# Performance work log

Measured on AMD Instinct MI355X. Metric: run time of the kernel, lower is better.

## Reference

```python
import jax, jax.numpy as jnp
import numpy as np

CHEB_K = 3
DIM_IN = 2
HIDDEN = 64
EMBED_DIM = 10
NODE_NUM = 2048
BATCH = 32


def _gconv(x, supports, W, b, cheb_k=CHEB_K):
    # Chebyshev graph conv applied directly to x (equivalent to building
    # T_k(A) matrices then applying: T_k(A) x = 2 A T_{k-1}(A) x - T_{k-2}(A) x).
    xs = [x, jnp.einsum('nm,bmc->bnc', supports, x)]
    for _ in range(2, cheb_k):
        xs.append(2.0 * jnp.einsum('nm,bmc->bnc', supports, xs[-1]) - xs[-2])
    x_g = jnp.concatenate(xs, axis=-1)          # [B, N, cheb_k*C]
    return jnp.einsum('bni,io->bno', x_g, W) + b


def setup_inputs() -> dict:
    key = jax.random.key(0)
    ks = jax.random.split(key, 7)
    c_in = DIM_IN + HIDDEN                       # 66
    # xavier_normal-ish scale for weights
    def xavier(k, fan_in, fan_out):
        std = float(np.sqrt(2.0 / (fan_in + fan_out)))
        return jax.random.normal(k, (fan_in, fan_out), dtype=jnp.float32) * std
    return {
        'x': jax.random.normal(ks[0], (BATCH, NODE_NUM, DIM_IN), dtype=jnp.float32),
        'state': jax.random.normal(ks[1], (BATCH, NODE_NUM, HIDDEN), dtype=jnp.float32),
        'node_embeddings': jax.random.normal(ks[2], (NODE_NUM, EMBED_DIM), dtype=jnp.float32),
        'W_gate': xavier(ks[3], CHEB_K * c_in, 2 * HIDDEN),
        'b_gate': jnp.zeros((2 * HIDDEN,), dtype=jnp.float32),
        'W_update': xavier(ks[4], CHEB_K * c_in, HIDDEN),
        'b_update': jnp.zeros((HIDDEN,), dtype=jnp.float32),
    }


def reference(x, state, node_embeddings, W_gate, b_gate, W_update, b_update):
    # adaptive adjacency: softmax(relu(E E^T), axis=1)
    logits = jnp.einsum('nc,mc->nm', node_embeddings, node_embeddings)
    supports = jax.nn.softmax(jax.nn.relu(logits), axis=1)   # [N, N]

    input_and_state = jnp.concatenate([x, state], axis=-1)   # [B, N, dim_in+hidden]
    z_r = jax.nn.sigmoid(_gconv(input_and_state, supports, W_gate, b_gate))
    z, r = jnp.split(z_r, 2, axis=-1)                        # each [B, N, hidden]
    candidate = jnp.concatenate([x, z * state], axis=-1)
    hc = jnp.tanh(_gconv(candidate, supports, W_update, b_update))
    h = r * state + (1.0 - r) * hc
    return h
```

## Files before the change

kernel.cpp:

```cpp
#include <hip/hip_runtime.h>


typedef __bf16 bf16x8 __attribute__((ext_vector_type(8)));
typedef __bf16 bf16x4 __attribute__((ext_vector_type(4)));
typedef float  f32x4  __attribute__((ext_vector_type(4)));

#define GLB(p) ((__attribute__((address_space(1))) void*)(void*)(p))
#define LDS(p) ((__attribute__((address_space(3))) void*)(p))

__global__ void supports_kernel(const float* __restrict__ E, __bf16* __restrict__ S) {
    const int n = blockIdx.x;
    const int t = threadIdx.x;
    const int l = t & 63, w = t >> 6;
    float en[10];
#pragma unroll
    for (int i = 0; i < 10; ++i) en[i] = E[n * 10 + i];
    float vals[8];
    float mx = 0.f;
#pragma unroll
    for (int q = 0; q < 8; ++q) {
        const int m = q * 256 + t;
        const float* em = E + (size_t)m * 10;
        float d = 0.f;
#pragma unroll
        for (int i = 0; i < 10; ++i) d += en[i] * em[i];
        d = fmaxf(d, 0.f);
        vals[q] = d;
        mx = fmaxf(mx, d);
    }
#pragma unroll
    for (int off = 32; off; off >>= 1) mx = fmaxf(mx, __shfl_xor(mx, off));
    __shared__ float sm[4], ss[4];
    if (l == 0) sm[w] = mx;
    __syncthreads();
    mx = fmaxf(fmaxf(sm[0], sm[1]), fmaxf(sm[2], sm[3]));
    float sum = 0.f;
#pragma unroll
    for (int q = 0; q < 8; ++q) { vals[q] = __expf(vals[q] - mx); sum += vals[q]; }
#pragma unroll
    for (int off = 32; off; off >>= 1) sum += __shfl_xor(sum, off);
    if (l == 0) ss[w] = sum;
    __syncthreads();
    sum = ss[0] + ss[1] + ss[2] + ss[3];
    const float inv = 1.f / sum;
#pragma unroll
    for (int q = 0; q < 8; ++q) S[(size_t)n * 2048 + q * 256 + t] = (__bf16)(vals[q] * inv);
}

__global__ void zero_pad(__bf16* __restrict__ Tpad) {
    const int id = blockIdx.x * 256 + threadIdx.x;
    bf16x8 z;
#pragma unroll
    for (int j = 0; j < 8; ++j) z[j] = (__bf16)0.f;
    *(bf16x8*)&Tpad[(size_t)id * 8] = z;
}

__global__ __launch_bounds__(256, 2)
void build_t2(const float* __restrict__ x, const float* __restrict__ st,
              const __bf16* __restrict__ zr, __bf16* __restrict__ T) {
    __shared__ float Ls[66 * 129];
    const int b  = blockIdx.x >> 4;
    const int n0 = (blockIdx.x & 15) << 7;
    const int t = threadIdx.x;
    const size_t mb = (size_t)b * 2048 + n0;
    if (t < 128) {
        const float2 v = *(const float2*)&x[(mb + t) * 2];
        Ls[t] = v.x;
        Ls[129 + t] = v.y;
    }
#pragma unroll
    for (int r = 0; r < 8; ++r) {
        const int task = r * 256 + t;
        const int q = task & 15, n = task >> 4;
        f32x4 v = *(const f32x4*)&st[(mb + n) * 64 + q * 4];
        if (zr) {
            const bf16x4 z = *(const bf16x4*)&zr[(mb + n) * 128 + q * 4];
#pragma unroll
            for (int j = 0; j < 4; ++j) v[j] *= (float)z[j];
        }
        const int base = (2 + q * 4) * 129 + n;
#pragma unroll
        for (int j = 0; j < 4; ++j) Ls[base + j * 129] = v[j];
    }
    __syncthreads();
#pragma unroll
    for (int r = 0; r < 5; ++r) {
        const int task = r * 256 + t;
        if (task < 1056) {
            const int c = task >> 4, seg = task & 15;
            const float* src = &Ls[c * 129 + seg * 8];
            bf16x8 o;
#pragma unroll
            for (int j = 0; j < 8; ++j) o[j] = (__bf16)src[j];
            *(bf16x8*)&T[(size_t)(b * 66 + c) * 2048 + n0 + seg * 8] = o;
        }
    }
}

__global__ __launch_bounds__(256, 2)
void transpose_g(const __bf16* __restrict__ T0, const __bf16* __restrict__ T1,
                 const __bf16* __restrict__ T2, __bf16* __restrict__ G) {
    __shared__ __bf16 Ls[128 * 256];
    const int b  = blockIdx.x >> 4;
    const int n0 = (blockIdx.x & 15) << 7;
    const int t = threadIdx.x;
#pragma unroll
    for (int r = 0; r < 16; ++r) {
        const int task = r * 256 + t;
        const int k = task >> 4, seg = task & 15;
        bf16x8 v;
        if (k < 198) {
            const __bf16* T; int c;
            if (k < 66)       { T = T0; c = k; }
            else if (k < 132) { T = T1; c = k - 66; }
            else              { T = T2; c = k - 132; }
            v = *(const bf16x8*)&T[(size_t)(b * 66 + c) * 2048 + n0 + seg * 8];
        } else {
#pragma unroll
            for (int j = 0; j < 8; ++j) v[j] = (__bf16)0.f;
        }
        const int base = seg * 8 * 256 + (((k >> 3) ^ seg) << 3) + (k & 7);
#pragma unroll
        for (int j = 0; j < 8; ++j) Ls[base + j * 256] = v[j];
    }
    __syncthreads();
#pragma unroll
    for (int r = 0; r < 16; ++r) {
        const int task = r * 256 + t;
        const int m = task >> 5, c8 = task & 31;
        bf16x8 w = *(const bf16x8*)&Ls[m * 256 + ((c8 ^ (m >> 3)) << 3)];
        *(bf16x8*)&G[(size_t)(b * 2048 + n0 + m) * 256 + c8 * 8] = w;
    }
}

__global__ void build_wt(const float* __restrict__ W, __bf16* __restrict__ WT, int Nout) {
    const int id = blockIdx.x * 256 + threadIdx.x;
    const int o = id >> 8, k = id & 255;
    WT[id] = (o < Nout && k < 198) ? (__bf16)W[(size_t)k * Nout + o] : (__bf16)0.f;
}

__global__ __launch_bounds__(128, 3)
void gemm_s(const __bf16* __restrict__ A, int lda,
            const __bf16* __restrict__ Bt, int ldb,
            int K, int epi,
            __bf16* __restrict__ outT, const __bf16* __restrict__ subT,
            float* __restrict__ outF, const float* __restrict__ bias,
            __bf16* __restrict__ zrO, const __bf16* __restrict__ zrI,
            const float* __restrict__ state) {
    __shared__ __align__(16) __bf16 As[64 * 64];
    __shared__ __align__(16) __bf16 Bs[128 * 64];
    const int t = threadIdx.x;
    const int l = t & 63, w = t >> 6;
    const int lm = l & 15, kq = l >> 4;
    const int lm7 = lm & 7;
    const int m0 = blockIdx.x * 64;
    const int c0 = blockIdx.y * 128;
    const int sr = l >> 3;
    const int gsw = (l & 7) ^ sr;

    f32x4 acc[4][4];
#pragma unroll
    for (int i = 0; i < 4; ++i)
#pragma unroll
        for (int j = 0; j < 4; ++j) acc[i][j] = (f32x4)0.f;

    const __bf16* Asrc = A  + (size_t)(m0 + w * 32 + sr) * lda + gsw * 8;
    const __bf16* Bsrc = Bt + (size_t)(c0 + w * 64 + sr) * ldb + gsw * 8;
    __bf16* AsD = As + (w * 32) * 64 + l * 8;
    __bf16* BsD = Bs + (w * 64) * 64 + l * 8;

    for (int k0 = 0; k0 < K; k0 += 64) {
#pragma unroll
        for (int q = 0; q < 4; ++q)
            __builtin_amdgcn_global_load_lds(GLB(Asrc + (size_t)q * 8 * lda + k0),
                                             LDS(AsD + q * 8 * 64), 16, 0, 0);
#pragma unroll
        for (int q = 0; q < 8; ++q)
            __builtin_amdgcn_global_load_lds(GLB(Bsrc + (size_t)q * 8 * ldb + k0),
                                             LDS(BsD + q * 8 * 64), 16, 0, 0);
        __syncthreads();
#pragma unroll
        for (int ks = 0; ks < 2; ++ks) {
            const int ga = (((ks << 2) | kq) ^ lm7) << 3;
            bf16x8 af[4], bfr[4];
#pragma unroll
            for (int i = 0; i < 4; ++i)
                af[i] = *(const bf16x8*)(As + (i * 16 + lm) * 64 + ga);
#pragma unroll
            for (int j = 0; j < 4; ++j)
                bfr[j] = *(const bf16x8*)(Bs + (w * 64 + j * 16 + lm) * 64 + ga);
#pragma unroll
            for (int i = 0; i < 4; ++i)
#pragma unroll
                for (int j = 0; j < 4; ++j)
                    acc[i][j] = __builtin_amdgcn_mfma_f32_16x16x32_bf16(af[i], bfr[j], acc[i][j], 0, 0, 0);
        }
        __syncthreads();
    }

    const int rb0 = m0 + kq * 4;
    const int cb0 = c0 + w * 64 + lm;
#pragma unroll
    for (int i = 0; i < 4; ++i) {
        const int rbase = rb0 + i * 16;
#pragma unroll
        for (int j = 0; j < 4; ++j) {
            const int c = cb0 + j * 16;
            f32x4 v = acc[i][j];
            if (epi == 0) {
                bf16x4 pk;
#pragma unroll
                for (int r = 0; r < 4; ++r) pk[r] = (__bf16)v[r];
                *(bf16x4*)&outT[(size_t)c * 2048 + rbase] = pk;
            } else if (epi == 1) {
                bf16x4 s = *(const bf16x4*)&subT[(size_t)c * 2048 + rbase];
                bf16x4 pk;
#pragma unroll
                for (int r = 0; r < 4; ++r) pk[r] = (__bf16)(2.f * v[r] - (float)s[r]);
                *(bf16x4*)&outT[(size_t)c * 2048 + rbase] = pk;
            } else if (epi == 2) {
                const float bb = bias[c];
#pragma unroll
                for (int r = 0; r < 4; ++r) {
                    float xx = fminf(fmaxf(v[r] + bb, -30.f), 30.f);
                    zrO[(size_t)(rbase + r) * 128 + c] = (__bf16)(1.f / (1.f + __expf(-xx)));
                }
            } else {
                if (c < 64) {
                    const float bb = bias[c];
#pragma unroll
                    for (int r = 0; r < 4; ++r) {
                        const int m = rbase + r;
                        float xx = fminf(fmaxf(v[r] + bb, -15.f), 15.f);
                        float e = __expf(2.f * xx);
                        float hc = (e - 1.f) / (e + 1.f);
                        float rr = (float)zrI[(size_t)m * 128 + 64 + c];
                        float s = state[(size_t)m * 64 + c];
                        outF[(size_t)m * 64 + c] = rr * s + (1.f - rr) * hc;
                    }
                }
            }
        }
    }
}

extern "C" void kernel_launch(void* const* d_in, const int* in_sizes, int n_in,
                              void* d_out, int out_size, void* d_ws, size_t ws_size,
                              hipStream_t stream) {
    (void)in_sizes; (void)n_in; (void)out_size; (void)ws_size;
    const float* x  = (const float*)d_in[0];
    const float* st = (const float*)d_in[1];
    const float* E  = (const float*)d_in[2];
    const float* Wg = (const float*)d_in[3];
    const float* bg = (const float*)d_in[4];
    const float* Wu = (const float*)d_in[5];
    const float* bu = (const float*)d_in[6];
    float* out = (float*)d_out;

    char* p = (char*)d_ws;
    __bf16* S   = (__bf16*)p; p += (size_t)2048 * 2048 * 2;
    __bf16* T0  = (__bf16*)p; p += (size_t)2176 * 2048 * 2;
    __bf16* T1  = (__bf16*)p; p += (size_t)2176 * 2048 * 2;
    __bf16* T2  = (__bf16*)p; p += (size_t)2176 * 2048 * 2;
    __bf16* G   = (__bf16*)p; p += (size_t)65536 * 256 * 2;
    __bf16* ZR  = (__bf16*)p; p += (size_t)65536 * 128 * 2;
    __bf16* WTg = (__bf16*)p; p += 128 * 256 * 2;
    __bf16* WTu = (__bf16*)p; p += 128 * 256 * 2;

    build_wt<<<128, 256, 0, stream>>>(Wg, WTg, 128);
    build_wt<<<128, 256, 0, stream>>>(Wu, WTu, 64);
    zero_pad<<<64, 256, 0, stream>>>(T0 + (size_t)2112 * 2048);
    supports_kernel<<<2048, 256, 0, stream>>>(E, S);

    build_t2<<<512, 256, 0, stream>>>(x, st, nullptr, T0);
    gemm_s<<<dim3(32, 17), 128, 0, stream>>>(S, 2048, T0, 2048, 2048, 0, T1, nullptr, nullptr, nullptr, nullptr, nullptr, nullptr);
    gemm_s<<<dim3(32, 17), 128, 0, stream>>>(S, 2048, T1, 2048, 2048, 1, T2, T0, nullptr, nullptr, nullptr, nullptr, nullptr);
    transpose_g<<<512, 256, 0, stream>>>(T0, T1, T2, G);
    gemm_s<<<dim3(1024, 1), 128, 0, stream>>>(G, 256, WTg, 256, 256, 2, nullptr, nullptr, nullptr, bg, ZR, nullptr, nullptr);

    build_t2<<<512, 256, 0, stream>>>(x, st, ZR, T0);
    gemm_s<<<dim3(32, 17), 128, 0, stream>>>(S, 2048, T0, 2048, 2048, 0, T1, nullptr, nullptr, nullptr, nullptr, nullptr, nullptr);
    gemm_s<<<dim3(32, 17), 128, 0, stream>>>(S, 2048, T1, 2048, 2048, 1, T2, T0, nullptr, nullptr, nullptr, nullptr, nullptr);
    transpose_g<<<512, 256, 0, stream>>>(T0, T1, T2, G);
    gemm_s<<<dim3(1024, 1), 128, 0, stream>>>(G, 256, WTu, 256, 256, 3, nullptr, nullptr, out, bu, nullptr, ZR, st);
}
```

Before: 297.3 us.

## Replace GEMM with single-wave double-buffered 64x64 tile kernel and grid swizzle

Replaces the two-wave 64x128 GEMM with a one-wave kernel that computes a 64x64 tile. Global-to-LDS loads are double-buffered, so the next K slice loads while the current one feeds the MFMAs. Because the block is a single wave, explicit vmcnt waits and scheduling barriers replace __syncthreads. The supports GEMMs also get a swizzled 1D block order to improve L2 reuse of S and T tiles. The cost is fewer waves per block and more blocks, which could weaken latency hiding or raise redundant loads of the shared operand.

```diff
diff --git a/kernel.cpp b/kernel.cpp
--- a/kernel.cpp
+++ b/kernel.cpp
@@ -139,22 +139,28 @@
     WT[id] = (o < Nout && k < 198) ? (__bf16)W[(size_t)k * Nout + o] : (__bf16)0.f;
 }
 
-__global__ __launch_bounds__(128, 3)
-void gemm_s(const __bf16* __restrict__ A, int lda,
-            const __bf16* __restrict__ Bt, int ldb,
-            int K, int epi,
-            __bf16* __restrict__ outT, const __bf16* __restrict__ subT,
-            float* __restrict__ outF, const float* __restrict__ bias,
-            __bf16* __restrict__ zrO, const __bf16* __restrict__ zrI,
-            const float* __restrict__ state) {
-    __shared__ __align__(16) __bf16 As[64 * 64];
-    __shared__ __align__(16) __bf16 Bs[128 * 64];
-    const int t = threadIdx.x;
-    const int l = t & 63, w = t >> 6;
-    const int lm = l & 15, kq = l >> 4;
-    const int lm7 = lm & 7;
-    const int m0 = blockIdx.x * 64;
-    const int c0 = blockIdx.y * 128;
+__global__ __launch_bounds__(64, 2)
+void gemm_dw(const __bf16* __restrict__ A, int lda,
+             const __bf16* __restrict__ Bt, int ldb,
+             int K, int epi, int swz,
+             __bf16* __restrict__ outT, const __bf16* __restrict__ subT,
+             float* __restrict__ outF, const float* __restrict__ bias,
+             __bf16* __restrict__ zrO, const __bf16* __restrict__ zrI,
+             const float* __restrict__ state) {
+    __shared__ __align__(16) __bf16 As[2][64 * 64];
+    __shared__ __align__(16) __bf16 Bs[2][64 * 64];
+    int mt, ct;
+    if (swz) {
+        const int id = blockIdx.x;
+        mt = (id & 7) * 4 + ((id >> 3) & 3);
+        ct = id >> 5;
+    } else {
+        mt = blockIdx.x;
+        ct = blockIdx.y;
+    }
+    const int m0 = mt * 64, c0 = ct * 64;
+    const int l = threadIdx.x;
+    const int lm = l & 15, kq = l >> 4, lm7 = lm & 7;
     const int sr = l >> 3;
     const int gsw = (l & 7) ^ sr;
 
@@ -164,42 +170,57 @@
 #pragma unroll
         for (int j = 0; j < 4; ++j) acc[i][j] = (f32x4)0.f;
 
-    const __bf16* Asrc = A  + (size_t)(m0 + w * 32 + sr) * lda + gsw * 8;
-    const __bf16* Bsrc = Bt + (size_t)(c0 + w * 64 + sr) * ldb + gsw * 8;
-    __bf16* AsD = As + (w * 32) * 64 + l * 8;
-    __bf16* BsD = Bs + (w * 64) * 64 + l * 8;
-
-    for (int k0 = 0; k0 < K; k0 += 64) {
-#pragma unroll
-        for (int q = 0; q < 4; ++q)
+    const __bf16* Asrc = A  + (size_t)(m0 + sr) * lda + gsw * 8;
+    const __bf16* Bsrc = Bt + (size_t)(c0 + sr) * ldb + gsw * 8;
+    const int dst = l * 8;
+
+    auto stage = [&](int buf, int k0) {
+#pragma unroll
+        for (int q = 0; q < 8; ++q)
             __builtin_amdgcn_global_load_lds(GLB(Asrc + (size_t)q * 8 * lda + k0),
-                                             LDS(AsD + q * 8 * 64), 16, 0, 0);
+                                             LDS(&As[buf][q * 512 + dst]), 16, 0, 0);
 #pragma unroll
         for (int q = 0; q < 8; ++q)
             __builtin_amdgcn_global_load_lds(GLB(Bsrc + (size_t)q * 8 * ldb + k0),
-                                             LDS(BsD + q * 8 * 64), 16, 0, 0);
-        __syncthreads();
+                                             LDS(&Bs[buf][q * 512 + dst]), 16, 0, 0);
+    };
+    auto compute = [&](int buf) {
 #pragma unroll
         for (int ks = 0; ks < 2; ++ks) {
             const int ga = (((ks << 2) | kq) ^ lm7) << 3;
             bf16x8 af[4], bfr[4];
 #pragma unroll
             for (int i = 0; i < 4; ++i)
-                af[i] = *(const bf16x8*)(As + (i * 16 + lm) * 64 + ga);
+                af[i] = *(const bf16x8*)&As[buf][(i * 16 + lm) * 64 + ga];
 #pragma unroll
             for (int j = 0; j < 4; ++j)
-                bfr[j] = *(const bf16x8*)(Bs + (w * 64 + j * 16 + lm) * 64 + ga);
+                bfr[j] = *(const bf16x8*)&Bs[buf][(j * 16 + lm) * 64 + ga];
 #pragma unroll
             for (int i = 0; i < 4; ++i)
 #pragma unroll
                 for (int j = 0; j < 4; ++j)
                     acc[i][j] = __builtin_amdgcn_mfma_f32_16x16x32_bf16(af[i], bfr[j], acc[i][j], 0, 0, 0);
         }
-        __syncthreads();
-    }
+    };
+
+    stage(0, 0);
+    int buf = 0;
+    for (int k0 = 64; k0 < K; k0 += 64) {
+        stage(buf ^ 1, k0);
+        __builtin_amdgcn_sched_barrier(0);
+        __builtin_amdgcn_s_waitcnt(0x4F70);
+        __builtin_amdgcn_sched_barrier(0);
+        compute(buf);
+        __builtin_amdgcn_sched_barrier(0);
+        buf ^= 1;
+    }
+    __builtin_amdgcn_sched_barrier(0);
+    __builtin_amdgcn_s_waitcnt(0x0F70);
+    __builtin_amdgcn_sched_barrier(0);
+    compute(buf);
 
     const int rb0 = m0 + kq * 4;
-    const int cb0 = c0 + w * 64 + lm;
+    const int cb0 = c0 + lm;
 #pragma unroll
     for (int i = 0; i < 4; ++i) {
         const int rbase = rb0 + i * 16;
@@ -273,14 +294,14 @@
     supports_kernel<<<2048, 256, 0, stream>>>(E, S);
 
     build_t2<<<512, 256, 0, stream>>>(x, st, nullptr, T0);
-    gemm_s<<<dim3(32, 17), 128, 0, stream>>>(S, 2048, T0, 2048, 2048, 0, T1, nullptr, nullptr, nullptr, nullptr, nullptr, nullptr);
-    gemm_s<<<dim3(32, 17), 128, 0, stream>>>(S, 2048, T1, 2048, 2048, 1, T2, T0, nullptr, nullptr, nullptr, nullptr, nullptr);
+    gemm_dw<<<1088, 64, 0, stream>>>(S, 2048, T0, 2048, 2048, 0, 1, T1, nullptr, nullptr, nullptr, nullptr, nullptr, nullptr);
+    gemm_dw<<<1088, 64, 0, stream>>>(S, 2048, T1, 2048, 2048, 1, 1, T2, T0, nullptr, nullptr, nullptr, nullptr, nullptr);
     transpose_g<<<512, 256, 0, stream>>>(T0, T1, T2, G);
-    gemm_s<<<dim3(1024, 1), 128, 0, stream>>>(G, 256, WTg, 256, 256, 2, nullptr, nullptr, nullptr, bg, ZR, nullptr, nullptr);
+    gemm_dw<<<dim3(1024, 2), 64, 0, stream>>>(G, 256, WTg, 256, 256, 2, 0, nullptr, nullptr, nullptr, bg, ZR, nullptr, nullptr);
 
     build_t2<<<512, 256, 0, stream>>>(x, st, ZR, T0);
-    gemm_s<<<dim3(32, 17), 128, 0, stream>>>(S, 2048, T0, 2048, 2048, 0, T1, nullptr, nullptr, nullptr, nullptr, nullptr, nullptr);
-    gemm_s<<<dim3(32, 17), 128, 0, stream>>>(S, 2048, T1, 2048, 2048, 1, T2, T0, nullptr, nullptr, nullptr, nullptr, nullptr);
+    gemm_dw<<<1088, 64, 0, stream>>>(S, 2048, T0, 2048, 2048, 0, 1, T1, nullptr, nullptr, nullptr, nullptr, nullptr, nullptr);
+    gemm_dw<<<1088, 64, 0, stream>>>(S, 2048, T1, 2048, 2048, 1, 1, T2, T0, nullptr, nullptr, nullptr, nullptr, nullptr);
     transpose_g<<<512, 256, 0, stream>>>(T0, T1, T2, G);
-    gemm_s<<<dim3(1024, 1), 128, 0, stream>>>(G, 256, WTu, 256, 256, 3, nullptr, nullptr, out, bu, nullptr, ZR, st);
-}
+    gemm_dw<<<dim3(1024, 1), 64, 0, stream>>>(G, 256, WTu, 256, 256, 3, 0, nullptr, nullptr, out, bu, nullptr, ZR, st);
+}
```

New measurement: 421.6 us. 1.42x slower.
